# Performance work log

Hardware: AMD Instinct MI355X
Metric: run time of the kernel (lower is better)

Reference implementation:

```python
import jax, jax.numpy as jnp
import numpy as np
from jax import lax

N = 16384       # input points
STRIDE = 4
M = N // STRIDE # sampled centers (single batch: n_o = [o[0]//stride])
NSAMPLE = 16
CIN = 64
COUT = 128
EPS = 1e-5      # BatchNorm1d default eps


def setup_inputs() -> dict:
    key = jax.random.key(0)
    k1, k2, k3, k4 = jax.random.split(key, 4)
    p = jax.random.normal(k1, (N, 3), dtype=jnp.float32)
    n = jax.random.normal(k2, (N, 3), dtype=jnp.float32)
    x = jax.random.normal(k3, (N, CIN), dtype=jnp.float32)
    o = jnp.array([N], dtype=jnp.int32)  # single point cloud
    W = jax.random.normal(k4, (COUT, 3 + CIN), dtype=jnp.float32) * 0.05
    gamma = jnp.ones((COUT,), dtype=jnp.float32)
    beta = jnp.zeros((COUT,), dtype=jnp.float32)
    return {"p": p, "n": n, "x": x, "o": o, "W": W, "gamma": gamma, "beta": beta}


def _fps(p, m):
    """Furthest point sampling (pointops.furthestsampling), single batch."""
    npts = p.shape[0]
    def step(carry, _):
        dists, last = carry
        d = jnp.sum((p - p[last]) ** 2, axis=-1)
        dists = jnp.minimum(dists, d)
        nxt = jnp.argmax(dists).astype(jnp.int32)
        return (dists, nxt), nxt
    first = jnp.int32(0)
    init = (jnp.full((npts,), 1e10, dtype=p.dtype), first)
    _, rest = lax.scan(step, init, None, length=m - 1)
    return jnp.concatenate([first[None], rest])  # [m]


def reference(p, n, x, o, W, gamma, beta):
    # --- furthest sampling: n_o = [o[0]//stride] = [M] (static for single batch)
    idx = _fps(p, M)                      # [M] int32
    n_p = p[idx]                          # [M,3] new coords
    n_n = n[idx]                          # [M,3] new normals
    # --- queryandgroup: kNN of each center in full cloud, use_xyz=True
    d2 = (jnp.sum(n_p * n_p, -1)[:, None]
          + jnp.sum(p * p, -1)[None, :]
          - 2.0 * n_p @ p.T)              # [M,N]
    _, knn = lax.top_k(-lax.stop_gradient(d2), NSAMPLE)   # [M,NSAMPLE]
    grouped_xyz = p[knn] - n_p[:, None, :]                # [M,NS,3] relative coords
    grouped_x = x[knn]                                    # [M,NS,CIN]
    feat = jnp.concatenate([grouped_xyz, grouped_x], axis=-1)  # [M,NS,3+CIN]
    # --- linear (no bias) -> BN (training stats, per channel) -> ReLU -> max over neighbors
    y = jnp.einsum('msc,oc->mso', feat, W)                # [M,NS,COUT]
    mean = jnp.mean(y, axis=(0, 1))
    var = jnp.mean((y - mean) ** 2, axis=(0, 1))          # biased var (torch BN)
    y = (y - mean) * lax.rsqrt(var + EPS) * gamma + beta
    y = jax.nn.relu(y)
    y = jnp.max(y, axis=1)                                # MaxPool1d(nsample) -> [M,COUT]
    n_o = jnp.array([M], dtype=jnp.int32)
    return (n_p, n_n, y, n_o)
```

## Files before the change

kernel.cpp:

```cpp
#include <hip/hip_runtime.h>
#include <math.h>

#define N_PTS 16384
#define M_CTR 4096
#define NS 16
#define CIN 64
#define COUT 128
#define CFEAT 67
#define CPB 4
#define NCELL 4096
#define PPT 16

__device__ __forceinline__ void pmerge(unsigned long long& a1, unsigned long long& a2,
                                       unsigned long long b1, unsigned long long b2) {
    unsigned long long n1 = a1 > b1 ? a1 : b1;
    unsigned long long lo = a1 > b1 ? b1 : a1;
    unsigned long long m2 = a2 > b2 ? a2 : b2;
    a2 = lo > m2 ? lo : m2;
    a1 = n1;
}

#define DPP_TOP2(CTRL) do { \
    unsigned _o1lo = (unsigned)__builtin_amdgcn_update_dpp(0, (int)(unsigned)k1, CTRL, 0xF, 0xF, false); \
    unsigned _o1hi = (unsigned)__builtin_amdgcn_update_dpp(0, (int)(unsigned)(k1>>32), CTRL, 0xF, 0xF, false); \
    unsigned _o2lo = (unsigned)__builtin_amdgcn_update_dpp(0, (int)(unsigned)k2, CTRL, 0xF, 0xF, false); \
    unsigned _o2hi = (unsigned)__builtin_amdgcn_update_dpp(0, (int)(unsigned)(k2>>32), CTRL, 0xF, 0xF, false); \
    unsigned long long _b1 = ((unsigned long long)_o1hi << 32) | (unsigned long long)_o1lo; \
    unsigned long long _b2 = ((unsigned long long)_o2hi << 32) | (unsigned long long)_o2lo; \
    pmerge(k1, k2, _b1, _b2); \
} while (0)

#define DPP_SWEEP(M) M(0x111); M(0x112); M(0x114); M(0x118); M(0x142); M(0x143)

#define REPEAT16(M) M(0) M(1) M(2) M(3) M(4) M(5) M(6) M(7) \
                    M(8) M(9) M(10) M(11) M(12) M(13) M(14) M(15)

__global__ void init_kernel(int* __restrict__ cnt, int* __restrict__ fill)
{
    int i = blockIdx.x * blockDim.x + threadIdx.x;
    if (i < NCELL) { cnt[i] = 0; fill[i] = 0; }
}

__global__ __launch_bounds__(256) void bbox_kernel(const float* __restrict__ p,
                                                   float* __restrict__ gbb)
{
    int t = threadIdx.x, lane = t & 63, w = t >> 6;
    float mnx = 1e30f, mny = 1e30f, mnz = 1e30f;
    float mxx = -1e30f, mxy = -1e30f, mxz = -1e30f;
    for (int i = t; i < N_PTS; i += 256) {
        float x = p[i*3], y = p[i*3+1], z = p[i*3+2];
        mnx = fminf(mnx, x); mny = fminf(mny, y); mnz = fminf(mnz, z);
        mxx = fmaxf(mxx, x); mxy = fmaxf(mxy, y); mxz = fmaxf(mxz, z);
    }
    for (int m = 1; m < 64; m <<= 1) {
        mnx = fminf(mnx, __shfl_xor(mnx, m)); mny = fminf(mny, __shfl_xor(mny, m));
        mnz = fminf(mnz, __shfl_xor(mnz, m));
        mxx = fmaxf(mxx, __shfl_xor(mxx, m)); mxy = fmaxf(mxy, __shfl_xor(mxy, m));
        mxz = fmaxf(mxz, __shfl_xor(mxz, m));
    }
    __shared__ float s[4][6];
    if (lane == 0) { s[w][0]=mnx; s[w][1]=mny; s[w][2]=mnz; s[w][3]=mxx; s[w][4]=mxy; s[w][5]=mxz; }
    __syncthreads();
    if (t == 0) {
        gbb[0] = fminf(fminf(s[0][0], s[1][0]), fminf(s[2][0], s[3][0]));
        gbb[1] = fminf(fminf(s[0][1], s[1][1]), fminf(s[2][1], s[3][1]));
        gbb[2] = fminf(fminf(s[0][2], s[1][2]), fminf(s[2][2], s[3][2]));
        gbb[3] = fmaxf(fmaxf(s[0][3], s[1][3]), fmaxf(s[2][3], s[3][3]));
        gbb[4] = fmaxf(fmaxf(s[0][4], s[1][4]), fmaxf(s[2][4], s[3][4]));
        gbb[5] = fmaxf(fmaxf(s[0][5], s[1][5]), fmaxf(s[2][5], s[3][5]));
    }
}

__global__ void assign_kernel(const float* __restrict__ p, const float* __restrict__ gbb,
                              int* __restrict__ c_of, int* __restrict__ cnt)
{
    int i = blockIdx.x * blockDim.x + threadIdx.x;
    if (i >= N_PTS) return;
    float bx = gbb[0], by = gbb[1], bz = gbb[2];
    float sx = 15.9999f / fmaxf(gbb[3] - bx, 1e-20f);
    float sy = 15.9999f / fmaxf(gbb[4] - by, 1e-20f);
    float sz = 15.9999f / fmaxf(gbb[5] - bz, 1e-20f);
    float x = p[i*3], y = p[i*3+1], z = p[i*3+2];
    int ix = min(15, max(0, (int)((x - bx) * sx)));
    int iy = min(15, max(0, (int)((y - by) * sy)));
    int iz = min(15, max(0, (int)((z - bz) * sz)));
    int c = (ix << 8) | (iy << 4) | iz;
    c_of[i] = c;
    atomicAdd(&cnt[c], 1);
}

__global__ __launch_bounds__(1024) void prefix_kernel(const int* __restrict__ cnt,
                                                      int* __restrict__ start)
{
    __shared__ int a[1024];
    int t = threadIdx.x;
    int c0 = cnt[4*t], c1 = cnt[4*t+1], c2 = cnt[4*t+2], c3 = cnt[4*t+3];
    int s = c0 + c1 + c2 + c3;
    a[t] = s; __syncthreads();
    for (int off = 1; off < 1024; off <<= 1) {
        int u = (t >= off) ? a[t - off] : 0;
        __syncthreads();
        a[t] += u;
        __syncthreads();
    }
    int ex = a[t] - s;
    start[4*t]   = ex;
    start[4*t+1] = ex + c0;
    start[4*t+2] = ex + c0 + c1;
    start[4*t+3] = ex + c0 + c1 + c2;
}

__global__ void scatter_kernel(const float* __restrict__ p, const int* __restrict__ c_of,
                               const int* __restrict__ start, int* __restrict__ fill,
                               float4* __restrict__ sp)
{
    int i = blockIdx.x * blockDim.x + threadIdx.x;
    if (i >= N_PTS) return;
    int c = c_of[i];
    int pos = start[c] + atomicAdd(&fill[c], 1);
    sp[pos] = make_float4(p[i*3], p[i*3+1], p[i*3+2], __int_as_float(i));
}

__global__ __launch_bounds__(1024) void fps_kernel(const float* __restrict__ p,
                                                   const float4* __restrict__ sp,
                                                   int* __restrict__ sel)
{
    __shared__ unsigned long long skw1[16], skw2[16];
    __shared__ float bq[6];
    __shared__ int bnsel;

    const int t = threadIdx.x;
    const int lane = t & 63, wave = t >> 6;
    const int base = t << 4;

#define DECL(k) float ds##k = 1e10f;
    REPEAT16(DECL)
#undef DECL

    float bmnx = 1e30f, bmny = 1e30f, bmnz = 1e30f;
    float bmxx = -1e30f, bmxy = -1e30f, bmxz = -1e30f;
#define BBX(k) { float4 P = sp[base + k]; \
    bmnx = fminf(bmnx, P.x); bmny = fminf(bmny, P.y); bmnz = fminf(bmnz, P.z); \
    bmxx = fmaxf(bmxx, P.x); bmxy = fmaxf(bmxy, P.y); bmxz = fmaxf(bmxz, P.z); }
    REPEAT16(BBX)
#undef BBX

    float tmax = 1e10f;
    unsigned long long kc1 = 0ull, kc2 = 0ull;

    if (t == 0) sel[0] = 0;
    float q1x = p[0], q1y = p[1], q1z = p[2];
    float q2x = 0.f, q2y = 0.f, q2z = 0.f;
    bool two = false, first = true;
    __syncthreads();

    int it = 1;
    while (it < M_CTR) {
        bool act;
        if (first) act = true;
        else {
            float cm = tmax * 1.00001f;
            float ddx = fmaxf(fmaxf(__fsub_rn(bmnx, q1x), __fsub_rn(q1x, bmxx)), 0.f);
            float ddy = fmaxf(fmaxf(__fsub_rn(bmny, q1y), __fsub_rn(q1y, bmxy)), 0.f);
            float ddz = fmaxf(fmaxf(__fsub_rn(bmnz, q1z), __fsub_rn(q1z, bmxz)), 0.f);
            float dm1 = __fadd_rn(__fadd_rn(__fmul_rn(ddx,ddx), __fmul_rn(ddy,ddy)),
                                  __fmul_rn(ddz,ddz));
            act = dm1 < cm;
            if (!act && two) {
                float ex = fmaxf(fmaxf(__fsub_rn(bmnx, q2x), __fsub_rn(q2x, bmxx)), 0.f);
                float ey = fmaxf(fmaxf(__fsub_rn(bmny, q2y), __fsub_rn(q2y, bmxy)), 0.f);
                float ez = fmaxf(fmaxf(__fsub_rn(bmnz, q2z), __fsub_rn(q2z, bmxz)), 0.f);
                float dm2 = __fadd_rn(__fadd_rn(__fmul_rn(ex,ex), __fmul_rn(ey,ey)),
                                      __fmul_rn(ez,ez));
                act = dm2 < cm;
            }
        }
        unsigned long long wmask = __ballot(act);

        if (act) {
            float nmax = -1.0f;
            unsigned long long k1 = 0ull, k2 = 0ull;
#define UPD(k) { \
            float4 P = sp[base + k]; \
            float dx = __fsub_rn(P.x, q1x), dy = __fsub_rn(P.y, q1y), dz = __fsub_rn(P.z, q1z); \
            float d2 = __fadd_rn(__fadd_rn(__fmul_rn(dx,dx), __fmul_rn(dy,dy)), \
                                 __fmul_rn(dz,dz)); \
            float nd = fminf(ds##k, d2); \
            if (two) { \
                float ex = __fsub_rn(P.x, q2x), ey = __fsub_rn(P.y, q2y), ez = __fsub_rn(P.z, q2z); \
                float e2 = __fadd_rn(__fadd_rn(__fmul_rn(ex,ex), __fmul_rn(ey,ey)), \
                                     __fmul_rn(ez,ez)); \
                nd = fminf(nd, e2); \
            } \
            ds##k = nd; \
            nmax = fmaxf(nmax, nd); \
            unsigned long long kk = ((unsigned long long)__float_as_uint(nd) << 32) \
                                  | (unsigned long long)(~(unsigned)__float_as_int(P.w)); \
            if (kk > k1) { k2 = k1; k1 = kk; } else if (kk > k2) { k2 = kk; } }
            REPEAT16(UPD)
#undef UPD
            tmax = nmax;
            kc1 = k1; kc2 = k2;
        }

        if (wmask != 0ull) {
            unsigned long long k1 = kc1, k2 = kc2;
            DPP_SWEEP(DPP_TOP2);
            if (lane == 63) { skw1[wave] = k1; skw2[wave] = k2; }
        }
        __syncthreads();

        if (wave == 0) {
            unsigned long long k1 = (lane < 16) ? skw1[lane] : 0ull;
            unsigned long long k2 = (lane < 16) ? skw2[lane] : 0ull;
            DPP_SWEEP(DPP_TOP2);
            if (lane == 63) {
                unsigned long long A1 = k1, A2 = k2;
                int s1 = (int)(~(unsigned)(A1 & 0xFFFFFFFFull));
                int s2 = (int)(~(unsigned)(A2 & 0xFFFFFFFFull));
                sel[it] = s1;
                float nq1x = p[s1*3+0], nq1y = p[s1*3+1], nq1z = p[s1*3+2];
                float bx2 = p[s2*3+0], by2 = p[s2*3+1], bz2 = p[s2*3+2];
                int nsel = 1;
                if (A2 != 0ull && it + 1 < M_CTR) {
                    float dx = __fsub_rn(bx2, nq1x), dy = __fsub_rn(by2, nq1y), dz = __fsub_rn(bz2, nq1z);
                    float d2b = __fadd_rn(__fadd_rn(__fmul_rn(dx,dx), __fmul_rn(dy,dy)),
                                          __fmul_rn(dz,dz));
                    float db = __uint_as_float((unsigned)(A2 >> 32));
                    if (d2b >= db) { nsel = 2; sel[it + 1] = s2; }
                }
                bq[0] = nq1x; bq[1] = nq1y; bq[2] = nq1z;
                bq[3] = bx2;  bq[4] = by2;  bq[5] = bz2;
                bnsel = nsel;
            }
        }
        __syncthreads();
        int nsel = bnsel;
        q1x = bq[0]; q1y = bq[1]; q1z = bq[2];
        two = (nsel == 2);
        if (two) { q2x = bq[3]; q2y = bq[4]; q2z = bq[5]; }
        first = false;
        it += nsel;
    }
}

__global__ void prep_kernel(const float* __restrict__ p, const float* __restrict__ nrm,
                            const int* __restrict__ sel, float* __restrict__ pp2,
                            float* __restrict__ out)
{
    int i = blockIdx.x * blockDim.x + threadIdx.x;
    if (i < N_PTS) {
        float x = p[i*3], y = p[i*3+1], z = p[i*3+2];
        pp2[i] = __fadd_rn(__fadd_rn(__fmul_rn(x,x), __fmul_rn(y,y)), __fmul_rn(z,z));
    }
    if (i < M_CTR) {
        int j = sel[i];
        out[i*3+0] = p[j*3+0]; out[i*3+1] = p[j*3+1]; out[i*3+2] = p[j*3+2];
        out[12288 + i*3+0] = nrm[j*3+0];
        out[12288 + i*3+1] = nrm[j*3+1];
        out[12288 + i*3+2] = nrm[j*3+2];
    }
    if (i == 0) out[548864] = (float)M_CTR;
}

__global__ __launch_bounds__(256) void knn_kernel(const float* __restrict__ p,
                                                  const float* __restrict__ pp2,
                                                  const float* __restrict__ np ,
                                                  int* __restrict__ knn)
{
    const int lane = threadIdx.x & 63;
    const int wave = threadIdx.x >> 6;
    const int c = blockIdx.x * 4 + wave;

    float cx = np[c*3], cy = np[c*3+1], cz = np[c*3+2];
    float c2 = __fadd_rn(__fadd_rn(__fmul_rn(cx,cx), __fmul_rn(cy,cy)), __fmul_rn(cz,cz));

    float hd[16]; int hi[16];
#pragma unroll
    for (int k = 0; k < 16; ++k) { hd[k] = 1e30f; hi[k] = 0x7fffffff; }

    for (int t = 0; t < N_PTS/64; ++t) {
        int j = t*64 + lane;
        float px = p[j*3+0], py = p[j*3+1], pz = p[j*3+2];
        float dot = __fadd_rn(__fadd_rn(__fmul_rn(cx,px), __fmul_rn(cy,py)),
                              __fmul_rn(cz,pz));
        float d2  = __fsub_rn(__fadd_rn(c2, pp2[j]), __fmul_rn(2.0f, dot));
        if (d2 < hd[15]) {
#pragma unroll
            for (int k = 15; k >= 1; --k) {
                bool up   = d2 < hd[k-1];
                bool here = d2 < hd[k];
                hd[k] = up ? hd[k-1] : (here ? d2 : hd[k]);
                hi[k] = up ? hi[k-1] : (here ? j  : hi[k]);
            }
            if (d2 < hd[0]) { hd[0] = d2; hi[0] = j; }
        }
    }

    for (int r = 0; r < 16; ++r) {
        float wv = hd[0]; int wi = hi[0];
#pragma unroll
        for (int m = 1; m < 64; m <<= 1) {
            float ov = __shfl_xor(wv, m);
            int   oi = __shfl_xor(wi, m);
            bool b = (ov < wv) || (ov == wv && oi < wi);
            wv = b ? ov : wv; wi = b ? oi : wi;
        }
        if (hi[0] == wi) {
            knn[c*16 + r] = wi;
#pragma unroll
            for (int k = 0; k < 15; ++k) { hd[k] = hd[k+1]; hi[k] = hi[k+1]; }
            hd[15] = 1e30f; hi[15] = 0x7fffffff;
        }
    }
}

__global__ __launch_bounds__(128) void passA_kernel(const float* __restrict__ p,
                                                    const float* __restrict__ xf,
                                                    const float* __restrict__ W,
                                                    const int* __restrict__ knn,
                                                    const float* __restrict__ out ,
                                                    float* __restrict__ ymax,
                                                    float* __restrict__ ymin,
                                                    float* __restrict__ partials)
{
    __shared__ float Wt[CFEAT][COUT];
    __shared__ float ft[CPB][NS][CFEAT];
    __shared__ float bsum[CPB][COUT], bssq[CPB][COUT];

    const int t = threadIdx.x;
    const int mbase = blockIdx.x * CPB;

    for (int c = 0; c < CFEAT; ++c) Wt[c][t] = W[t*CFEAT + c];

    {
        int r = t >> 1, half = t & 1;
        int ci = r >> 4, s = r & 15;
        int m = mbase + ci;
        int nb = knn[m*NS + s];
        if (half == 0) {
            ft[ci][s][0] = __fsub_rn(p[nb*3+0], out[m*3+0]);
            ft[ci][s][1] = __fsub_rn(p[nb*3+1], out[m*3+1]);
            ft[ci][s][2] = __fsub_rn(p[nb*3+2], out[m*3+2]);
        }
        for (int c = half*32; c < half*32 + 32; ++c)
            ft[ci][s][3+c] = xf[nb*CIN + c];
    }
    __syncthreads();

    const int ci = t >> 5, l = t & 31;
    float acc[NS][4];
#pragma unroll
    for (int s = 0; s < NS; ++s) { acc[s][0]=0.f; acc[s][1]=0.f; acc[s][2]=0.f; acc[s][3]=0.f; }

    for (int c = 0; c < CFEAT; ++c) {
        float w0 = Wt[c][l], w1 = Wt[c][l+32], w2 = Wt[c][l+64], w3 = Wt[c][l+96];
#pragma unroll
        for (int s = 0; s < NS; ++s) {
            float f = ft[ci][s][c];
            acc[s][0] = fmaf(f, w0, acc[s][0]);
            acc[s][1] = fmaf(f, w1, acc[s][1]);
            acc[s][2] = fmaf(f, w2, acc[s][2]);
            acc[s][3] = fmaf(f, w3, acc[s][3]);
        }
    }

    const int m = mbase + ci;
#pragma unroll
    for (int j = 0; j < 4; ++j) {
        int o = l + 32*j;
        float s = 0.f, q = 0.f, mx = -1e30f, mn = 1e30f;
#pragma unroll
        for (int sidx = 0; sidx < NS; ++sidx) {
            float v = acc[sidx][j];
            s += v; q = fmaf(v, v, q);
            mx = fmaxf(mx, v); mn = fminf(mn, v);
        }
        bsum[ci][o] = s;
        bssq[ci][o] = q;
        ymax[m*COUT + o] = mx;
        ymin[m*COUT + o] = mn;
    }
    __syncthreads();
    if (t < COUT) {
        float s = bsum[0][t] + bsum[1][t] + bsum[2][t] + bsum[3][t];
        float q = bssq[0][t] + bssq[1][t] + bssq[2][t] + bssq[3][t];
        partials[t*1024          + blockIdx.x] = s;
        partials[(COUT + t)*1024 + blockIdx.x] = q;
    }
}

__global__ __launch_bounds__(256) void bnstat_kernel(const float* __restrict__ partials,
                                                     const float* __restrict__ gamma,
                                                     const float* __restrict__ beta,
                                                     float* __restrict__ scaleshift)
{
    __shared__ float red[256];
    int t = threadIdx.x;
    const float4* v4 = (const float4*)(partials + t*1024);
    float s = 0.f;
    for (int i = 0; i < 256; ++i) {
        float4 v = v4[i];
        s += v.x; s += v.y; s += v.z; s += v.w;
    }
    red[t] = s;
    __syncthreads();
    if (t < COUT) {
        const float inv = 1.0f / 65536.0f;
        float mean = red[t] * inv;
        float var  = red[COUT + t] * inv - mean*mean;
        float rstd = rsqrtf(var + 1e-5f);
        float g = gamma[t] * rstd;
        scaleshift[t]        = g;
        scaleshift[COUT + t] = beta[t] - mean * g;
    }
}

__global__ void final_kernel(float* __restrict__ y,
                             const float* __restrict__ ymin,
                             const float* __restrict__ scaleshift)
{
    int i = blockIdx.x * blockDim.x + threadIdx.x;
    if (i >= M_CTR * COUT) return;
    int o = i & (COUT - 1);
    float a = scaleshift[o], b = scaleshift[COUT + o];
    float v = (a >= 0.f) ? y[i] : ymin[i];
    float z = fmaf(a, v, b);
    y[i] = fmaxf(z, 0.f);
}

extern "C" void kernel_launch(void* const* d_in, const int* in_sizes, int n_in,
                              void* d_out, int out_size, void* d_ws, size_t ws_size,
                              hipStream_t stream)
{
    const float* p     = (const float*)d_in[0];
    const float* nrm   = (const float*)d_in[1];
    const float* xf    = (const float*)d_in[2];
    const float* W     = (const float*)d_in[4];
    const float* gamma = (const float*)d_in[5];
    const float* beta  = (const float*)d_in[6];

    float* out = (float*)d_out;
    char* ws = (char*)d_ws;
    int*   sel        = (int*)(ws + 0);
    float* pp2        = (float*)(ws + 16384);
    int*   knn        = (int*)(ws + 81920);
    float* ymin       = (float*)(ws + 344064);
    float* partials   = (float*)(ws + 2441216);
    float* scaleshift = (float*)(ws + 3489792);

    float4*   sp        = (float4*)(ws + 81920);
    char*     yb        = ws + 344064;
    int*      c_of      = (int*)(yb + 65536);
    int*      cellcnt   = (int*)(yb + 131072);
    int*      cellfill  = (int*)(yb + 147456);
    int*      cellstart = (int*)(yb + 163840);
    float*    gbb       = (float*)(yb + 180224);

    float* ymax = out + 24576;

    init_kernel   <<<16, 256, 0, stream>>>(cellcnt, cellfill);
    bbox_kernel   <<<1,  256, 0, stream>>>(p, gbb);
    assign_kernel <<<64, 256, 0, stream>>>(p, gbb, c_of, cellcnt);
    prefix_kernel <<<1,  1024, 0, stream>>>(cellcnt, cellstart);
    scatter_kernel<<<64, 256, 0, stream>>>(p, c_of, cellstart, cellfill, sp);
    fps_kernel    <<<1,  1024, 0, stream>>>(p, sp, sel);
    prep_kernel   <<<64, 256, 0, stream>>>(p, nrm, sel, pp2, out);
    knn_kernel    <<<1024, 256, 0, stream>>>(p, pp2, out, knn);
    passA_kernel  <<<M_CTR/CPB, 128, 0, stream>>>(p, xf, W, knn, out, ymax, ymin, partials);
    bnstat_kernel <<<1, 256, 0, stream>>>(partials, gamma, beta, scaleshift);
    final_kernel  <<<2048, 256, 0, stream>>>(ymax, ymin, scaleshift);
}
```

Baseline: 6.761 ms.

## Restructure FPS kernel: 512 threads, LDS distances, Morton cells, one barrier per step

The single-block furthest point sampling kernel now runs 512 threads with 32 points each. Per-point min distances move from registers into a 16K-float LDS array, and points are stored transposed so accesses coalesce. Candidate coordinates travel with the top-2 keys through the DPP reduction, and every thread redundantly merges the 8 wave results from double-buffered shared memory. This removes the second barrier and the global coordinate reload per iteration. Grid cells are also reordered by Morton code for tighter per-thread bounding boxes, at the cost of extra LDS traffic and wider DPP shuffles.

```diff
diff --git a/kernel.cpp b/kernel.cpp
--- a/kernel.cpp
+++ b/kernel.cpp
@@ -9,31 +9,44 @@
 #define CFEAT 67
 #define CPB 4
 #define NCELL 4096
-#define PPT 16
-
-__device__ __forceinline__ void pmerge(unsigned long long& a1, unsigned long long& a2,
-                                       unsigned long long b1, unsigned long long b2) {
-    unsigned long long n1 = a1 > b1 ? a1 : b1;
-    unsigned long long lo = a1 > b1 ? b1 : a1;
-    unsigned long long m2 = a2 > b2 ? a2 : b2;
-    a2 = lo > m2 ? lo : m2;
-    a1 = n1;
-}
-
-#define DPP_TOP2(CTRL) do { \
-    unsigned _o1lo = (unsigned)__builtin_amdgcn_update_dpp(0, (int)(unsigned)k1, CTRL, 0xF, 0xF, false); \
-    unsigned _o1hi = (unsigned)__builtin_amdgcn_update_dpp(0, (int)(unsigned)(k1>>32), CTRL, 0xF, 0xF, false); \
-    unsigned _o2lo = (unsigned)__builtin_amdgcn_update_dpp(0, (int)(unsigned)k2, CTRL, 0xF, 0xF, false); \
-    unsigned _o2hi = (unsigned)__builtin_amdgcn_update_dpp(0, (int)(unsigned)(k2>>32), CTRL, 0xF, 0xF, false); \
-    unsigned long long _b1 = ((unsigned long long)_o1hi << 32) | (unsigned long long)_o1lo; \
-    unsigned long long _b2 = ((unsigned long long)_o2hi << 32) | (unsigned long long)_o2lo; \
-    pmerge(k1, k2, _b1, _b2); \
+#define NTH 512
+#define PPT 32
+
+typedef unsigned long long u64;
+
+__device__ __forceinline__ void pmergeP(u64& a1, u64& a2,
+                                        float& x1, float& y1, float& z1,
+                                        float& x2, float& y2, float& z2,
+                                        u64 b1, u64 b2,
+                                        float dx1, float dy1, float dz1,
+                                        float dx2, float dy2, float dz2)
+{
+    bool t = b1 > a1;
+    u64 hi = t ? b1 : a1; float hx = t ? dx1 : x1, hy = t ? dy1 : y1, hz = t ? dz1 : z1;
+    u64 lo = t ? a1 : b1; float lx = t ? x1 : dx1, ly = t ? y1 : dy1, lz = t ? z1 : dz1;
+    bool u = b2 > a2;
+    u64 m  = u ? b2 : a2; float mx = u ? dx2 : x2, my = u ? dy2 : y2, mz = u ? dz2 : z2;
+    bool v = lo > m;
+    a2 = v ? lo : m; x2 = v ? lx : mx; y2 = v ? ly : my; z2 = v ? lz : mz;
+    a1 = hi; x1 = hx; y1 = hy; z1 = hz;
+}
+
+#define DPP_F(CTRL, x) __int_as_float(__builtin_amdgcn_update_dpp(0, __float_as_int(x), CTRL, 0xF, 0xF, false))
+
+#define SWEEP_STEP(CTRL) do { \
+    unsigned _b1lo = (unsigned)__builtin_amdgcn_update_dpp(0, (int)(unsigned)k1, CTRL, 0xF, 0xF, false); \
+    unsigned _b1hi = (unsigned)__builtin_amdgcn_update_dpp(0, (int)(unsigned)(k1>>32), CTRL, 0xF, 0xF, false); \
+    unsigned _b2lo = (unsigned)__builtin_amdgcn_update_dpp(0, (int)(unsigned)k2, CTRL, 0xF, 0xF, false); \
+    unsigned _b2hi = (unsigned)__builtin_amdgcn_update_dpp(0, (int)(unsigned)(k2>>32), CTRL, 0xF, 0xF, false); \
+    u64 _b1 = ((u64)_b1hi << 32) | (u64)_b1lo; \
+    u64 _b2 = ((u64)_b2hi << 32) | (u64)_b2lo; \
+    float _d1x = DPP_F(CTRL, c1x), _d1y = DPP_F(CTRL, c1y), _d1z = DPP_F(CTRL, c1z); \
+    float _d2x = DPP_F(CTRL, c2x), _d2y = DPP_F(CTRL, c2y), _d2z = DPP_F(CTRL, c2z); \
+    pmergeP(k1, k2, c1x, c1y, c1z, c2x, c2y, c2z, _b1, _b2, _d1x, _d1y, _d1z, _d2x, _d2y, _d2z); \
 } while (0)
 
-#define DPP_SWEEP(M) M(0x111); M(0x112); M(0x114); M(0x118); M(0x142); M(0x143)
-
-#define REPEAT16(M) M(0) M(1) M(2) M(3) M(4) M(5) M(6) M(7) \
-                    M(8) M(9) M(10) M(11) M(12) M(13) M(14) M(15)
+#define SWEEP_ALL SWEEP_STEP(0x111); SWEEP_STEP(0x112); SWEEP_STEP(0x114); \
+                  SWEEP_STEP(0x118); SWEEP_STEP(0x142); SWEEP_STEP(0x143)
 
 __global__ void init_kernel(int* __restrict__ cnt, int* __restrict__ fill)
 {
@@ -71,6 +84,9 @@
     }
 }
 
+__device__ __forceinline__ int part3_4(int v) {
+    return (v & 1) | ((v & 2) << 2) | ((v & 4) << 4) | ((v & 8) << 6);
+}
 __global__ void assign_kernel(const float* __restrict__ p, const float* __restrict__ gbb,
                               int* __restrict__ c_of, int* __restrict__ cnt)
 {
@@ -84,7 +100,7 @@
     int ix = min(15, max(0, (int)((x - bx) * sx)));
     int iy = min(15, max(0, (int)((y - by) * sy)));
     int iz = min(15, max(0, (int)((z - bz) * sz)));
-    int c = (ix << 8) | (iy << 4) | iz;
+    int c = (part3_4(ix) << 2) | (part3_4(iy) << 1) | part3_4(iz);
     c_of[i] = c;
     atomicAdd(&cnt[c], 1);
 }
@@ -112,46 +128,49 @@
 
 __global__ void scatter_kernel(const float* __restrict__ p, const int* __restrict__ c_of,
                                const int* __restrict__ start, int* __restrict__ fill,
-                               float4* __restrict__ sp)
+                               float4* __restrict__ spT)
 {
     int i = blockIdx.x * blockDim.x + threadIdx.x;
     if (i >= N_PTS) return;
     int c = c_of[i];
-    int pos = start[c] + atomicAdd(&fill[c], 1);
-    sp[pos] = make_float4(p[i*3], p[i*3+1], p[i*3+2], __int_as_float(i));
-}
-
-__global__ __launch_bounds__(1024) void fps_kernel(const float* __restrict__ p,
-                                                   const float4* __restrict__ sp,
-                                                   int* __restrict__ sel)
-{
-    __shared__ unsigned long long skw1[16], skw2[16];
-    __shared__ float bq[6];
-    __shared__ int bnsel;
+    int j = start[c] + atomicAdd(&fill[c], 1);
+    spT[(j & 31) * NTH + (j >> 5)] = make_float4(p[i*3], p[i*3+1], p[i*3+2], __int_as_float(i));
+}
+
+__global__ __launch_bounds__(NTH) void fps_kernel(const float* __restrict__ p,
+                                                  const float4* __restrict__ spT,
+                                                  int* __restrict__ sel)
+{
+    __shared__ float distT[N_PTS];
+    __shared__ u64 skw1[2][8], skw2[2][8];
+    __shared__ float skc[2][8][6];
 
     const int t = threadIdx.x;
     const int lane = t & 63, wave = t >> 6;
-    const int base = t << 4;
-
-#define DECL(k) float ds##k = 1e10f;
-    REPEAT16(DECL)
-#undef DECL
+
+    for (int i = t; i < N_PTS; i += NTH) distT[i] = 1e10f;
 
     float bmnx = 1e30f, bmny = 1e30f, bmnz = 1e30f;
     float bmxx = -1e30f, bmxy = -1e30f, bmxz = -1e30f;
-#define BBX(k) { float4 P = sp[base + k]; \
-    bmnx = fminf(bmnx, P.x); bmny = fminf(bmny, P.y); bmnz = fminf(bmnz, P.z); \
-    bmxx = fmaxf(bmxx, P.x); bmxy = fmaxf(bmxy, P.y); bmxz = fmaxf(bmxz, P.z); }
-    REPEAT16(BBX)
-#undef BBX
+#pragma unroll 8
+    for (int k = 0; k < PPT; ++k) {
+        float4 P = spT[(k << 9) + t];
+        bmnx = fminf(bmnx, P.x); bmny = fminf(bmny, P.y); bmnz = fminf(bmnz, P.z);
+        bmxx = fmaxf(bmxx, P.x); bmxy = fmaxf(bmxy, P.y); bmxz = fmaxf(bmxz, P.z);
+    }
 
     float tmax = 1e10f;
-    unsigned long long kc1 = 0ull, kc2 = 0ull;
+    u64 kc1 = 0ull, kc2 = 0ull;
+    float cc1x = 0.f, cc1y = 0.f, cc1z = 0.f;
+    float cc2x = 0.f, cc2y = 0.f, cc2z = 0.f;
+    u64 wk1 = 0ull, wk2 = 0ull;
+    float w1x = 0.f, w1y = 0.f, w1z = 0.f, w2x = 0.f, w2y = 0.f, w2z = 0.f;
 
     if (t == 0) sel[0] = 0;
     float q1x = p[0], q1y = p[1], q1z = p[2];
     float q2x = 0.f, q2y = 0.f, q2z = 0.f;
     bool two = false, first = true;
+    int rpar = 0;
     __syncthreads();
 
     int it = 1;
@@ -175,72 +194,94 @@
                 act = dm2 < cm;
             }
         }
-        unsigned long long wmask = __ballot(act);
 
         if (act) {
             float nmax = -1.0f;
-            unsigned long long k1 = 0ull, k2 = 0ull;
-#define UPD(k) { \
-            float4 P = sp[base + k]; \
-            float dx = __fsub_rn(P.x, q1x), dy = __fsub_rn(P.y, q1y), dz = __fsub_rn(P.z, q1z); \
-            float d2 = __fadd_rn(__fadd_rn(__fmul_rn(dx,dx), __fmul_rn(dy,dy)), \
-                                 __fmul_rn(dz,dz)); \
-            float nd = fminf(ds##k, d2); \
-            if (two) { \
-                float ex = __fsub_rn(P.x, q2x), ey = __fsub_rn(P.y, q2y), ez = __fsub_rn(P.z, q2z); \
-                float e2 = __fadd_rn(__fadd_rn(__fmul_rn(ex,ex), __fmul_rn(ey,ey)), \
-                                     __fmul_rn(ez,ez)); \
-                nd = fminf(nd, e2); \
-            } \
-            ds##k = nd; \
-            nmax = fmaxf(nmax, nd); \
-            unsigned long long kk = ((unsigned long long)__float_as_uint(nd) << 32) \
-                                  | (unsigned long long)(~(unsigned)__float_as_int(P.w)); \
-            if (kk > k1) { k2 = k1; k1 = kk; } else if (kk > k2) { k2 = kk; } }
-            REPEAT16(UPD)
-#undef UPD
+            u64 k1 = 0ull, k2 = 0ull;
+            float p1x = 0.f, p1y = 0.f, p1z = 0.f, p2x = 0.f, p2y = 0.f, p2z = 0.f;
+#pragma unroll 4
+            for (int k = 0; k < PPT; ++k) {
+                int a = (k << 9) + t;
+                float4 P = spT[a];
+                float D = distT[a];
+                float dx = __fsub_rn(P.x, q1x), dy = __fsub_rn(P.y, q1y), dz = __fsub_rn(P.z, q1z);
+                float d2 = __fadd_rn(__fadd_rn(__fmul_rn(dx,dx), __fmul_rn(dy,dy)),
+                                     __fmul_rn(dz,dz));
+                float nd = fminf(D, d2);
+                if (two) {
+                    float ex = __fsub_rn(P.x, q2x), ey = __fsub_rn(P.y, q2y), ez = __fsub_rn(P.z, q2z);
+                    float e2 = __fadd_rn(__fadd_rn(__fmul_rn(ex,ex), __fmul_rn(ey,ey)),
+                                         __fmul_rn(ez,ez));
+                    nd = fminf(nd, e2);
+                }
+                distT[a] = nd;
+                nmax = fmaxf(nmax, nd);
+                u64 kk = ((u64)__float_as_uint(nd) << 32)
+                       | (u64)(~(unsigned)__float_as_int(P.w));
+                bool g1 = kk > k1;
+                bool g2 = kk > k2;
+                u64 nk2 = g1 ? k1 : (g2 ? kk : k2);
+                float n2x = g1 ? p1x : (g2 ? P.x : p2x);
+                float n2y = g1 ? p1y : (g2 ? P.y : p2y);
+                float n2z = g1 ? p1z : (g2 ? P.z : p2z);
+                k1 = g1 ? kk : k1;
+                p1x = g1 ? P.x : p1x; p1y = g1 ? P.y : p1y; p1z = g1 ? P.z : p1z;
+                k2 = nk2; p2x = n2x; p2y = n2y; p2z = n2z;
+            }
             tmax = nmax;
             kc1 = k1; kc2 = k2;
-        }
-
+            cc1x = p1x; cc1y = p1y; cc1z = p1z;
+            cc2x = p2x; cc2y = p2y; cc2z = p2z;
+        }
+
+        unsigned long long wmask = __ballot(act);
         if (wmask != 0ull) {
-            unsigned long long k1 = kc1, k2 = kc2;
-            DPP_SWEEP(DPP_TOP2);
-            if (lane == 63) { skw1[wave] = k1; skw2[wave] = k2; }
+            u64 k1 = kc1, k2 = kc2;
+            float c1x = cc1x, c1y = cc1y, c1z = cc1z;
+            float c2x = cc2x, c2y = cc2y, c2z = cc2z;
+            SWEEP_ALL;
+            if (lane == 63) {
+                wk1 = k1; wk2 = k2;
+                w1x = c1x; w1y = c1y; w1z = c1z;
+                w2x = c2x; w2y = c2y; w2z = c2z;
+            }
+        }
+        if (lane == 63) {
+            skw1[rpar][wave] = wk1; skw2[rpar][wave] = wk2;
+            skc[rpar][wave][0] = w1x; skc[rpar][wave][1] = w1y; skc[rpar][wave][2] = w1z;
+            skc[rpar][wave][3] = w2x; skc[rpar][wave][4] = w2y; skc[rpar][wave][5] = w2z;
         }
         __syncthreads();
 
-        if (wave == 0) {
-            unsigned long long k1 = (lane < 16) ? skw1[lane] : 0ull;
-            unsigned long long k2 = (lane < 16) ? skw2[lane] : 0ull;
-            DPP_SWEEP(DPP_TOP2);
-            if (lane == 63) {
-                unsigned long long A1 = k1, A2 = k2;
-                int s1 = (int)(~(unsigned)(A1 & 0xFFFFFFFFull));
-                int s2 = (int)(~(unsigned)(A2 & 0xFFFFFFFFull));
-                sel[it] = s1;
-                float nq1x = p[s1*3+0], nq1y = p[s1*3+1], nq1z = p[s1*3+2];
-                float bx2 = p[s2*3+0], by2 = p[s2*3+1], bz2 = p[s2*3+2];
-                int nsel = 1;
-                if (A2 != 0ull && it + 1 < M_CTR) {
-                    float dx = __fsub_rn(bx2, nq1x), dy = __fsub_rn(by2, nq1y), dz = __fsub_rn(bz2, nq1z);
-                    float d2b = __fadd_rn(__fadd_rn(__fmul_rn(dx,dx), __fmul_rn(dy,dy)),
-                                          __fmul_rn(dz,dz));
-                    float db = __uint_as_float((unsigned)(A2 >> 32));
-                    if (d2b >= db) { nsel = 2; sel[it + 1] = s2; }
-                }
-                bq[0] = nq1x; bq[1] = nq1y; bq[2] = nq1z;
-                bq[3] = bx2;  bq[4] = by2;  bq[5] = bz2;
-                bnsel = nsel;
-            }
-        }
-        __syncthreads();
-        int nsel = bnsel;
-        q1x = bq[0]; q1y = bq[1]; q1z = bq[2];
+        u64 A1 = skw1[rpar][0], A2 = skw2[rpar][0];
+        float a1x = skc[rpar][0][0], a1y = skc[rpar][0][1], a1z = skc[rpar][0][2];
+        float a2x = skc[rpar][0][3], a2y = skc[rpar][0][4], a2z = skc[rpar][0][5];
+#pragma unroll
+        for (int w = 1; w < 8; ++w) {
+            pmergeP(A1, A2, a1x, a1y, a1z, a2x, a2y, a2z,
+                    skw1[rpar][w], skw2[rpar][w],
+                    skc[rpar][w][0], skc[rpar][w][1], skc[rpar][w][2],
+                    skc[rpar][w][3], skc[rpar][w][4], skc[rpar][w][5]);
+        }
+
+        int nsel = 1;
+        if (A2 != 0ull && it + 1 < M_CTR) {
+            float dx = __fsub_rn(a2x, a1x), dy = __fsub_rn(a2y, a1y), dz = __fsub_rn(a2z, a1z);
+            float d2b = __fadd_rn(__fadd_rn(__fmul_rn(dx,dx), __fmul_rn(dy,dy)),
+                                  __fmul_rn(dz,dz));
+            float db = __uint_as_float((unsigned)(A2 >> 32));
+            if (d2b >= db) nsel = 2;
+        }
+        if (t == 0) {
+            sel[it] = (int)(~(unsigned)(A1 & 0xFFFFFFFFull));
+            if (nsel == 2) sel[it + 1] = (int)(~(unsigned)(A2 & 0xFFFFFFFFull));
+        }
+        q1x = a1x; q1y = a1y; q1z = a1z;
         two = (nsel == 2);
-        if (two) { q2x = bq[3]; q2y = bq[4]; q2z = bq[5]; }
+        if (two) { q2x = a2x; q2y = a2y; q2z = a2z; }
         first = false;
         it += nsel;
+        rpar ^= 1;
     }
 }
 
@@ -449,7 +490,7 @@
     float* partials   = (float*)(ws + 2441216);
     float* scaleshift = (float*)(ws + 3489792);
 
-    float4*   sp        = (float4*)(ws + 81920);
+    float4*   spT       = (float4*)(ws + 81920);
     char*     yb        = ws + 344064;
     int*      c_of      = (int*)(yb + 65536);
     int*      cellcnt   = (int*)(yb + 131072);
@@ -463,8 +504,8 @@
     bbox_kernel   <<<1,  256, 0, stream>>>(p, gbb);
     assign_kernel <<<64, 256, 0, stream>>>(p, gbb, c_of, cellcnt);
     prefix_kernel <<<1,  1024, 0, stream>>>(cellcnt, cellstart);
-    scatter_kernel<<<64, 256, 0, stream>>>(p, c_of, cellstart, cellfill, sp);
-    fps_kernel    <<<1,  1024, 0, stream>>>(p, sp, sel);
+    scatter_kernel<<<64, 256, 0, stream>>>(p, c_of, cellstart, cellfill, spT);
+    fps_kernel    <<<1,  NTH, 0, stream>>>(p, spT, sel);
     prep_kernel   <<<64, 256, 0, stream>>>(p, nrm, sel, pp2, out);
     knn_kernel    <<<1024, 256, 0, stream>>>(p, pp2, out, knn);
     passA_kernel  <<<M_CTR/CPB, 128, 0, stream>>>(p, xf, W, knn, out, ymax, ymin, partials);
```

Result: slower. 17.12 ms (+153.2%).
